# Kernel optimization log

Measured on AMD Instinct MI355X. Metric: run time of the kernel, lower is better.

The kernel has to match this reference:

```python
import jax, jax.numpy as jnp
import numpy as np

DIM = 1024
HEADS = 16
DIM_HEAD = 64
INNER = HEADS * DIM_HEAD
EPS = 1e-5

def layernorm(x, g, b):
    mu = jnp.mean(x, axis=-1, keepdims=True)
    var = jnp.var(x, axis=-1, keepdims=True)
    return (x - mu) * jax.lax.rsqrt(var + EPS) * g + b

def setup_inputs() -> dict:
    key = jax.random.key(0)
    ks = jax.random.split(key, 9)
    b, t, n, m = 8, 8, 576, 64
    x = jax.random.normal(ks[0], (b, t, n, DIM), dtype=jnp.float32)
    latents = jax.random.normal(ks[1], (b, t, m, DIM), dtype=jnp.float32)
    att_mask = jax.random.randint(ks[2], (b, t, n), 0, 2, dtype=jnp.int32)
    s = 1.0 / np.sqrt(DIM)
    Wq = jax.random.normal(ks[3], (DIM, INNER), dtype=jnp.float32) * s
    Wkv = jax.random.normal(ks[4], (DIM, 2 * INNER), dtype=jnp.float32) * s
    Wo = jax.random.normal(ks[5], (INNER, DIM), dtype=jnp.float32) * (1.0 / np.sqrt(INNER))
    gm = jnp.ones((DIM,), jnp.float32); bm = jnp.zeros((DIM,), jnp.float32)
    gl = jnp.ones((DIM,), jnp.float32); bl = jnp.zeros((DIM,), jnp.float32)
    return {"x": x, "latents": latents, "att_mask": att_mask,
            "gm": gm, "bm": bm, "gl": gl, "bl": bl,
            "Wq": Wq, "Wkv": Wkv, "Wo": Wo}

def reference(x, latents, att_mask, gm, bm, gl, bl, Wq, Wkv, Wo):
    b, t, n, d = x.shape
    m = latents.shape[2]
    h, dh = HEADS, DIM_HEAD
    scale = dh ** -0.5

    xn = layernorm(x, gm, bm)
    ln = layernorm(latents, gl, bl)

    q = ln @ Wq                                  # b t m inner
    kv_input = jnp.concatenate((xn, ln), axis=-2)  # b t (n+m) d
    kv = kv_input @ Wkv                          # b t (n+m) 2*inner
    k, v = jnp.split(kv, 2, axis=-1)

    # b t s (h dh) -> b h t s dh
    def split_heads(a):
        bb, tt, ss, _ = a.shape
        return a.reshape(bb, tt, ss, h, dh).transpose(0, 3, 1, 2, 4)
    q = split_heads(q) * scale
    k = split_heads(k)
    v = split_heads(v)

    sim = jnp.einsum('bhtid,bhtjd->bhtij', q, k)   # b h t m (n+m)

    # mask: concat ones for latent KV positions; broadcast over heads and query dim
    full_mask = jnp.concatenate(
        [att_mask.astype(sim.dtype), jnp.ones((b, t, m), sim.dtype)], axis=2)  # b t (n+m)
    neg = jnp.finfo(sim.dtype).min
    bias = jnp.where(full_mask > 0, 0.0, neg)      # b t (n+m)
    sim = sim + bias[:, None, :, None, :]

    attn = jax.nn.softmax(sim, axis=-1)
    out = jnp.einsum('bhtij,bhtjd->bhtid', attn, v)  # b h t m dh
    out = out.transpose(0, 2, 3, 1, 4).reshape(b, t, m, h * dh)
    return out @ Wo
```

## Files before the change

kernel.cpp:

```cpp
#include <hip/hip_runtime.h>
#include <hip/hip_bf16.h>
#include <stdint.h>

#define NCTX 576
#define MLAT 64
#define SEQ 640
#define DMODEL 1024
#define NH 16
#define INNER_ 1024
#define KV_W 2048

typedef float f32x4 __attribute__((ext_vector_type(4)));
typedef __bf16 bf16x8 __attribute__((ext_vector_type(8)));
typedef unsigned short u16;
typedef unsigned int u32;
typedef unsigned long long u64;

typedef __attribute__((address_space(1))) u32 as1_u32;
typedef __attribute__((address_space(3))) u32 as3_u32;

__device__ __forceinline__ u16 f2bf(float f) {
    u32 u = __builtin_bit_cast(u32, f);
    u32 r = (u + 0x7fffu + ((u >> 16) & 1u)) >> 16;
    return (u16)r;
}

__device__ __forceinline__ int xcd_swizzle(int orig, int nwg) {
    int q = nwg >> 3, r = nwg & 7;
    int xcd = orig & 7, loc = orig >> 3;
    return (xcd < r ? xcd * (q + 1) : r * (q + 1) + (xcd - r) * q) + loc;
}

__global__ __launch_bounds__(640) void build_idx(const int* __restrict__ mask,
                                                 int* __restrict__ sidx,
                                                 int* __restrict__ cnt,
                                                 int* __restrict__ latst) {
    int bt = blockIdx.x, tid = threadIdx.x;
    __shared__ int ps[640];
    int valid = (tid < NCTX) ? (mask[bt * NCTX + tid] > 0 ? 1 : 0) : 0;
    ps[tid] = valid;
    __syncthreads();
    for (int off = 1; off < 640; off <<= 1) {
        int v = (tid >= off) ? ps[tid - off] : 0;
        __syncthreads();
        ps[tid] += v;
        __syncthreads();
    }
    int nc = ps[NCTX - 1];
    if (valid) sidx[bt * SEQ + ps[tid] - 1] = tid;
    if (tid < MLAT) sidx[bt * SEQ + nc + tid] = NCTX + tid;
    if (tid == 0) { cnt[bt] = nc + MLAT; latst[bt] = nc; }
}

__global__ __launch_bounds__(256) void transpose_cast_all(const float* __restrict__ Wq,
                                                          const float* __restrict__ Wkv,
                                                          const float* __restrict__ Wo,
                                                          u16* __restrict__ WqT,
                                                          u16* __restrict__ WkvT,
                                                          u16* __restrict__ WoT) {
    __shared__ float tile[64][65];
    int id = blockIdx.x;
    const float* src; u16* dst; int N;
    if (id < 256)      { src = Wq;  dst = WqT;  N = 1024; }
    else if (id < 768) { src = Wkv; dst = WkvT; N = 2048; id -= 256; }
    else               { src = Wo;  dst = WoT;  N = 1024; id -= 768; }
    int nx = N >> 6;
    int n0 = (id % nx) * 64, k0 = (id / nx) * 64;
    int tid = threadIdx.x;
#pragma unroll
    for (int i = 0; i < 4; ++i) {
        int idx = i * 256 + tid;
        int kk = idx >> 4;
        int nn = (idx & 15) << 2;
        float4 v = *(const float4*)(src + (u64)(k0 + kk) * N + n0 + nn);
        tile[kk][nn] = v.x; tile[kk][nn + 1] = v.y; tile[kk][nn + 2] = v.z; tile[kk][nn + 3] = v.w;
    }
    __syncthreads();
#pragma unroll
    for (int i = 0; i < 4; ++i) {
        int idx = i * 256 + tid;
        int nn = idx >> 4;
        int kk = (idx & 15) << 2;
        ushort4 o;
        o.x = f2bf(tile[kk][nn]);     o.y = f2bf(tile[kk + 1][nn]);
        o.z = f2bf(tile[kk + 2][nn]); o.w = f2bf(tile[kk + 3][nn]);
        *(ushort4*)(dst + (u64)(n0 + nn) * 1024 + k0 + kk) = o;
    }
}

__global__ __launch_bounds__(256) void ln_cast(const float* __restrict__ x,
                                               const float* __restrict__ lat,
                                               const float* __restrict__ gm, const float* __restrict__ bm,
                                               const float* __restrict__ gl, const float* __restrict__ bl,
                                               u16* __restrict__ out,
                                               const int* __restrict__ sidx, const int* __restrict__ cnt,
                                               int bt0, int nrows) {
    int w = threadIdx.x >> 6, lane = threadIdx.x & 63;
    int nw = gridDim.x * 4;
    for (int row = blockIdx.x * 4 + w; row < nrows; row += nw) {
        int btl = row / SEQ, jl = row - btl * SEQ;
        int btg = bt0 + btl;
        if (jl >= cnt[btg]) continue;
        int sp = sidx[btg * SEQ + jl];
        const float *src, *g, *b;
        if (sp < NCTX) { src = x + ((u64)btl * NCTX + sp) * DMODEL; g = gm; b = bm; }
        else           { src = lat + ((u64)btl * MLAT + (sp - NCTX)) * DMODEL; g = gl; b = bl; }
        float4 v[4];
        float sum = 0.f, sq = 0.f;
#pragma unroll
        for (int j = 0; j < 4; ++j) {
            v[j] = *(const float4*)(src + ((j * 64 + lane) << 2));
            sum += v[j].x + v[j].y + v[j].z + v[j].w;
            sq  += v[j].x * v[j].x + v[j].y * v[j].y + v[j].z * v[j].z + v[j].w * v[j].w;
        }
#pragma unroll
        for (int off = 1; off < 64; off <<= 1) {
            sum += __shfl_xor(sum, off, 64);
            sq  += __shfl_xor(sq, off, 64);
        }
        float mu = sum * (1.0f / DMODEL);
        float var = sq * (1.0f / DMODEL) - mu * mu;
        float rstd = rsqrtf(var + 1e-5f);
        u16* orow = out + (u64)row * DMODEL;
#pragma unroll
        for (int j = 0; j < 4; ++j) {
            float4 gv = *(const float4*)(g + ((j * 64 + lane) << 2));
            float4 bv = *(const float4*)(b + ((j * 64 + lane) << 2));
            ushort4 o;
            o.x = f2bf((v[j].x - mu) * rstd * gv.x + bv.x);
            o.y = f2bf((v[j].y - mu) * rstd * gv.y + bv.y);
            o.z = f2bf((v[j].z - mu) * rstd * gv.z + bv.z);
            o.w = f2bf((v[j].w - mu) * rstd * gv.w + bv.w);
            *(ushort4*)(orow + ((j * 64 + lane) << 2)) = o;
        }
    }
}

template <int VT_SPLIT, typename OUT_T>
__global__ __launch_bounds__(512) void gemm256(const u16* __restrict__ A,
                                               const u16* __restrict__ Bt,
                                               OUT_T* __restrict__ C, u16* __restrict__ vt,
                                               int M, int ldc, float scale,
                                               const int* __restrict__ cntp, int bt0) {
    constexpr int K = 1024;
    constexpr int BK = 64;
    constexpr int NT = K / BK;
    __shared__ u16 As[2][256 * BK];
    __shared__ u16 Bs[2][256 * BK];
    int tid = threadIdx.x;
    int lane = tid & 63;
    int w = tid >> 6;
    int wm = w >> 2, wn = w & 3;
    int nwg = gridDim.x * gridDim.y;
    int wg = xcd_swizzle(blockIdx.y * gridDim.x + blockIdx.x, nwg);
    int m0 = (wg / gridDim.x) * 256;
    int n0 = (wg % gridDim.x) * 256;

    if (cntp) {
        int btile = m0 / SEQ, off = m0 - btile * SEQ;
        if (off + 256 <= SEQ && off >= cntp[bt0 + btile]) return;
    }

    int rl = lane & 15, cgl = lane >> 4;

    auto stage = [&](int t, int buf) {
        int k0 = t * BK;
#pragma unroll
        for (int i = 0; i < 4; ++i) {
            int r = i * 64 + (tid >> 3);
            int cg = tid & 7;
            int col = (cg ^ (r & 7)) << 3;
            __builtin_amdgcn_global_load_lds((const as1_u32*)(A + (u64)(m0 + r) * K + k0 + col),
                (as3_u32*)(&As[buf][0] + ((i * 512 + (w << 6)) << 3)), 16, 0, 0);
            __builtin_amdgcn_global_load_lds((const as1_u32*)(Bt + (u64)(n0 + r) * K + k0 + col),
                (as3_u32*)(&Bs[buf][0] + ((i * 512 + (w << 6)) << 3)), 16, 0, 0);
        }
    };

    f32x4 acc[8][4] = {};

    stage(0, 0);
    stage(1, 1);
    asm volatile("s_waitcnt vmcnt(8)" ::: "memory");
    __builtin_amdgcn_s_barrier();
    __builtin_amdgcn_sched_barrier(0);

#pragma unroll 1
    for (int t = 0; t < NT; ++t) {
        int buf = t & 1;
        const u16* Ab = &As[buf][0];
        const u16* Bb = &Bs[buf][0];
#pragma unroll
        for (int qd = 0; qd < 4; ++qd) {
            const int mh = qd & 1, nh = qd >> 1;
            bf16x8 a[2][4], b[2][2];
#pragma unroll
            for (int kk = 0; kk < 2; ++kk) {
#pragma unroll
                for (int mi = 0; mi < 4; ++mi) {
                    int r = wm * 128 + (mh * 4 + mi) * 16 + rl;
                    int c = kk * 4 + cgl;
                    a[kk][mi] = *(const bf16x8*)(Ab + r * BK + ((c ^ (r & 7)) << 3));
                }
#pragma unroll
                for (int ni = 0; ni < 2; ++ni) {
                    int r = wn * 64 + (nh * 2 + ni) * 16 + rl;
                    int c = kk * 4 + cgl;
                    b[kk][ni] = *(const bf16x8*)(Bb + r * BK + ((c ^ (r & 7)) << 3));
                }
            }
            __builtin_amdgcn_s_setprio(1);
#pragma unroll
            for (int kk = 0; kk < 2; ++kk)
#pragma unroll
                for (int mi = 0; mi < 4; ++mi)
#pragma unroll
                    for (int ni = 0; ni < 2; ++ni)
                        acc[mh * 4 + mi][nh * 2 + ni] = __builtin_amdgcn_mfma_f32_16x16x32_bf16(
                            a[kk][mi], b[kk][ni], acc[mh * 4 + mi][nh * 2 + ni], 0, 0, 0);
            __builtin_amdgcn_s_setprio(0);
        }
        __builtin_amdgcn_sched_barrier(0);
        __builtin_amdgcn_s_barrier();
        __builtin_amdgcn_sched_barrier(0);
        if (t + 2 < NT) {
            stage(t + 2, buf);
            asm volatile("s_waitcnt vmcnt(8)" ::: "memory");
        } else {
            asm volatile("s_waitcnt vmcnt(0)" ::: "memory");
        }
        __builtin_amdgcn_s_barrier();
        __builtin_amdgcn_sched_barrier(0);
    }

    if (VT_SPLIT && n0 >= INNER_) {
#pragma unroll
        for (int mi = 0; mi < 8; ++mi) {
            int grow = m0 + wm * 128 + mi * 16 + cgl * 4;
            int bt = grow / SEQ;
            int s = grow - bt * SEQ;
#pragma unroll
            for (int ni = 0; ni < 4; ++ni) {
                int vcol = (n0 - INNER_) + wn * 64 + ni * 16 + rl;
                ushort4 o;
                o.x = f2bf(acc[mi][ni][0] * scale);
                o.y = f2bf(acc[mi][ni][1] * scale);
                o.z = f2bf(acc[mi][ni][2] * scale);
                o.w = f2bf(acc[mi][ni][3] * scale);
                *(ushort4*)(vt + ((u64)bt * INNER_ + vcol) * SEQ + s) = o;
            }
        }
    } else {
#pragma unroll
        for (int mi = 0; mi < 8; ++mi) {
#pragma unroll
            for (int r = 0; r < 4; ++r) {
                int grow = m0 + wm * 128 + mi * 16 + cgl * 4 + r;
#pragma unroll
                for (int ni = 0; ni < 4; ++ni) {
                    int gcol = n0 + wn * 64 + ni * 16 + rl;
                    float val = acc[mi][ni][r] * scale;
                    if constexpr (sizeof(OUT_T) == 2)
                        C[(u64)grow * ldc + gcol] = (OUT_T)f2bf(val);
                    else
                        C[(u64)grow * ldc + gcol] = val;
                }
            }
        }
    }
}

template <typename OUT_T>
__global__ __launch_bounds__(256) void gemm_bf16(const u16* __restrict__ A,
                                                 const u16* __restrict__ Bt,
                                                 OUT_T* __restrict__ C,
                                                 int M, int ldc, float scale,
                                                 const int* __restrict__ latstart, int bt0) {
    constexpr int K = 1024;
    __shared__ u16 As[128 * 32];
    __shared__ u16 Bs[128 * 32];
    int tid = threadIdx.x;
    int lane = tid & 63;
    int w = tid >> 6;
    int wm = w >> 1, wn = w & 1;
    int nwg = gridDim.x * gridDim.y;
    int wg = xcd_swizzle(blockIdx.y * gridDim.x + blockIdx.x, nwg);
    int m0 = (wg / gridDim.x) * 128;
    int n0 = (wg % gridDim.x) * 128;

    f32x4 acc[4][4] = {};

    for (int k0 = 0; k0 < K; k0 += 32) {
        __syncthreads();
#pragma unroll
        for (int i = 0; i < 2; ++i) {
            int t = i * 256 + tid;
            int r = t >> 2;
            int cg = t & 3;
            int col = (cg ^ ((r >> 1) & 3)) << 3;
            int grow = m0 + r; if (grow >= M) grow = M - 1;
            u64 row;
            if (latstart) {
                int lbt = grow >> 6;
                row = (u64)lbt * SEQ + latstart[bt0 + lbt] + (grow & 63);
            } else {
                row = (u64)grow;
            }
            const u16* ga = A + row * K + k0 + col;
            __builtin_amdgcn_global_load_lds((const as1_u32*)ga,
                (as3_u32*)(As + ((i * 256 + (w << 6)) << 3)), 16, 0, 0);
            const u16* gb = Bt + (u64)(n0 + r) * K + k0 + col;
            __builtin_amdgcn_global_load_lds((const as1_u32*)gb,
                (as3_u32*)(Bs + ((i * 256 + (w << 6)) << 3)), 16, 0, 0);
        }
        __syncthreads();
        bf16x8 a[4], b[4];
        int rl = lane & 15;
        int cgl = lane >> 4;
#pragma unroll
        for (int mi = 0; mi < 4; ++mi) {
            int r = wm * 64 + mi * 16 + rl;
            int c = (cgl ^ ((r >> 1) & 3)) << 3;
            a[mi] = *(const bf16x8*)(As + r * 32 + c);
        }
#pragma unroll
        for (int ni = 0; ni < 4; ++ni) {
            int r = wn * 64 + ni * 16 + rl;
            int c = (cgl ^ ((r >> 1) & 3)) << 3;
            b[ni] = *(const bf16x8*)(Bs + r * 32 + c);
        }
#pragma unroll
        for (int mi = 0; mi < 4; ++mi)
#pragma unroll
            for (int ni = 0; ni < 4; ++ni)
                acc[mi][ni] = __builtin_amdgcn_mfma_f32_16x16x32_bf16(a[mi], b[ni], acc[mi][ni], 0, 0, 0);
    }
    int rl = lane & 15, rg = lane >> 4;
#pragma unroll
    for (int mi = 0; mi < 4; ++mi) {
#pragma unroll
        for (int r = 0; r < 4; ++r) {
            int grow = m0 + wm * 64 + mi * 16 + rg * 4 + r;
            if (grow < M) {
#pragma unroll
                for (int ni = 0; ni < 4; ++ni) {
                    int gcol = n0 + wn * 64 + ni * 16 + rl;
                    float val = acc[mi][ni][r] * scale;
                    if constexpr (sizeof(OUT_T) == 2)
                        C[(u64)grow * ldc + gcol] = (OUT_T)f2bf(val);
                    else
                        C[(u64)grow * ldc + gcol] = val;
                }
            }
        }
    }
}

__global__ __launch_bounds__(256) void attn_kernel(const u16* __restrict__ qb,
                                                   const u16* __restrict__ kbuf,
                                                   const u16* __restrict__ vtb,
                                                   const int* __restrict__ cnt,
                                                   u16* __restrict__ ob, int bt0) {
    int h = blockIdx.x;
    int btl = blockIdx.y;
    int tid = threadIdx.x, lane = tid & 63, w = tid >> 6;
    __shared__ u16 Ks[2][64 * 64];
    __shared__ u16 Vs[2][64 * 64];
    __shared__ u16 Ps[4][16 * 64];
    __shared__ float bias_s[2][64];
    int rl = lane & 15, cgl = lane >> 4;

    int cn = cnt[bt0 + btl];
    int nch = (cn + 63) >> 6;

    bf16x8 aq[2];
    {
        int qr = btl * MLAT + w * 16 + rl;
        const u16* qp = qb + (u64)qr * INNER_ + h * 64 + cgl * 8;
        aq[0] = *(const bf16x8*)(qp);
        aq[1] = *(const bf16x8*)(qp + 32);
    }
    f32x4 acc[4] = {};
    float mrow[4], lrow[4];
#pragma unroll
    for (int r = 0; r < 4; ++r) { mrow[r] = -1e30f; lrow[r] = 0.f; }

    const u16* kbase = kbuf + (u64)btl * SEQ * INNER_ + h * 64;
    const u16* vbase = vtb + ((u64)btl * INNER_ + h * 64) * SEQ;

    auto stage = [&](int c, int bf) {
#pragma unroll
        for (int i = 0; i < 2; ++i) {
            int t = i * 256 + tid;
            int r = t >> 3, cg = t & 7;
            int col = (cg ^ (r & 7)) << 3;
            __builtin_amdgcn_global_load_lds((const as1_u32*)(kbase + (u64)(c * 64 + r) * INNER_ + col),
                (as3_u32*)(&Ks[bf][0] + ((i * 256 + (w << 6)) << 3)), 16, 0, 0);
            __builtin_amdgcn_global_load_lds((const as1_u32*)(vbase + (u64)r * SEQ + c * 64 + col),
                (as3_u32*)(&Vs[bf][0] + ((i * 256 + (w << 6)) << 3)), 16, 0, 0);
        }
        if (tid < 64) {
            int pos = c * 64 + tid;
            bias_s[bf][tid] = (pos < cn) ? 0.f : -1e30f;
        }
    };

    stage(0, 0);
    __syncthreads();

    for (int c = 0; c < nch; ++c) {
        int bf = c & 1;
        if (c + 1 < nch) stage(c + 1, bf ^ 1);

        f32x4 sf[4];
        __builtin_amdgcn_s_setprio(1);
#pragma unroll
        for (int ni = 0; ni < 4; ++ni) {
            f32x4 z = {};
#pragma unroll
            for (int kk = 0; kk < 2; ++kk) {
                int r = ni * 16 + rl;
                int g = (kk * 4 + cgl) ^ (r & 7);
                bf16x8 bk = *(const bf16x8*)(&Ks[bf][0] + r * 64 + g * 8);
                z = __builtin_amdgcn_mfma_f32_16x16x32_bf16(aq[kk], bk, z, 0, 0, 0);
            }
            float bias = bias_s[bf][ni * 16 + rl];
            z[0] += bias; z[1] += bias; z[2] += bias; z[3] += bias;
            sf[ni] = z;
        }
        __builtin_amdgcn_s_setprio(0);
        float alpha[4];
#pragma unroll
        for (int r = 0; r < 4; ++r) {
            float m = fmaxf(fmaxf(sf[0][r], sf[1][r]), fmaxf(sf[2][r], sf[3][r]));
            m = fmaxf(m, __shfl_xor(m, 1, 64));
            m = fmaxf(m, __shfl_xor(m, 2, 64));
            m = fmaxf(m, __shfl_xor(m, 4, 64));
            m = fmaxf(m, __shfl_xor(m, 8, 64));
            float mn = fmaxf(mrow[r], m);
            alpha[r] = __expf(mrow[r] - mn);
            mrow[r] = mn;
        }
#pragma unroll
        for (int ni = 0; ni < 4; ++ni)
#pragma unroll
            for (int r = 0; r < 4; ++r)
                sf[ni][r] = __expf(sf[ni][r] - mrow[r]);
#pragma unroll
        for (int r = 0; r < 4; ++r) {
            float s = sf[0][r] + sf[1][r] + sf[2][r] + sf[3][r];
            s += __shfl_xor(s, 1, 64);
            s += __shfl_xor(s, 2, 64);
            s += __shfl_xor(s, 4, 64);
            s += __shfl_xor(s, 8, 64);
            lrow[r] = lrow[r] * alpha[r] + s;
        }
        u16* pw = Ps[w];
#pragma unroll
        for (int ni = 0; ni < 4; ++ni) {
#pragma unroll
            for (int r = 0; r < 4; ++r) {
                int qrow = cgl * 4 + r;
                int kcol = ni * 16 + rl;
                int cs = (((kcol >> 3) ^ (qrow & 7)) << 3) + (kcol & 7);
                pw[qrow * 64 + cs] = f2bf(sf[ni][r]);
            }
        }
#pragma unroll
        for (int oi = 0; oi < 4; ++oi)
#pragma unroll
            for (int r = 0; r < 4; ++r)
                acc[oi][r] *= alpha[r];
        bf16x8 ap[2];
#pragma unroll
        for (int kk = 0; kk < 2; ++kk) {
            int cc = (((kk * 4 + cgl) ^ (rl & 7)) << 3);
            ap[kk] = *(const bf16x8*)(pw + rl * 64 + cc);
        }
        __builtin_amdgcn_s_setprio(1);
#pragma unroll
        for (int oi = 0; oi < 4; ++oi) {
#pragma unroll
            for (int kk = 0; kk < 2; ++kk) {
                int r = oi * 16 + rl;
                int g = (kk * 4 + cgl) ^ (r & 7);
                bf16x8 bv = *(const bf16x8*)(&Vs[bf][0] + r * 64 + g * 8);
                acc[oi] = __builtin_amdgcn_mfma_f32_16x16x32_bf16(ap[kk], bv, acc[oi], 0, 0, 0);
            }
        }
        __builtin_amdgcn_s_setprio(0);
        __syncthreads();
    }
#pragma unroll
    for (int r = 0; r < 4; ++r) {
        float inv = 1.0f / lrow[r];
        int qrow = btl * MLAT + w * 16 + cgl * 4 + r;
        u16* op = ob + (u64)qrow * INNER_ + h * 64;
#pragma unroll
        for (int oi = 0; oi < 4; ++oi)
            op[oi * 16 + rl] = f2bf(acc[oi][r] * inv);
    }
}

extern "C" void kernel_launch(void* const* d_in, const int* in_sizes, int n_in,
                              void* d_out, int out_size, void* d_ws, size_t ws_size,
                              hipStream_t stream) {
    const float* x    = (const float*)d_in[0];
    const float* lat  = (const float*)d_in[1];
    const int*   am   = (const int*)d_in[2];
    const float* gm   = (const float*)d_in[3];
    const float* bm   = (const float*)d_in[4];
    const float* gl   = (const float*)d_in[5];
    const float* bl   = (const float*)d_in[6];
    const float* Wq   = (const float*)d_in[7];
    const float* Wkv  = (const float*)d_in[8];
    const float* Wo   = (const float*)d_in[9];
    float* out = (float*)d_out;

    int* sidx  = (int*)d_ws;
    int* cnt   = sidx + 64 * SEQ;
    int* latst = cnt + 64;
    u16* WqT   = (u16*)(latst + 64);
    u16* WkvT  = WqT + 1024 * 1024;
    u16* WoT   = WkvT + 2048 * 1024;
    u16* bufs  = WoT + 1024 * 1024;

    size_t fixed = (size_t)(64 * SEQ + 128) * 4 + (size_t)(1024 * 1024 + 2048 * 1024 + 1024 * 1024) * 2;
    size_t perbt = (size_t)(SEQ * DMODEL + SEQ * INNER_ + INNER_ * SEQ + MLAT * INNER_ + MLAT * INNER_) * 2;
    int C = 64;
    while (C > 1 && fixed + (size_t)C * perbt > ws_size) C >>= 1;

    build_idx<<<64, 640, 0, stream>>>(am, sidx, cnt, latst);
    transpose_cast_all<<<1024, 256, 0, stream>>>(Wq, Wkv, Wo, WqT, WkvT, WoT);

    for (int bt0 = 0; bt0 < 64; bt0 += C) {
        u16* xn  = bufs;
        u16* kb  = xn + (size_t)C * SEQ * DMODEL;
        u16* vtp = kb + (size_t)C * SEQ * INNER_;
        u16* qbp = vtp + (size_t)C * INNER_ * SEQ;
        u16* ao  = qbp + (size_t)C * MLAT * INNER_;

        ln_cast<<<2048, 256, 0, stream>>>(x + (u64)bt0 * NCTX * DMODEL,
                                          lat + (u64)bt0 * MLAT * DMODEL,
                                          gm, bm, gl, bl, xn, sidx, cnt, bt0, C * SEQ);
        gemm256<1, u16><<<dim3(KV_W / 256, (C * SEQ) / 256), 512, 0, stream>>>(
            xn, WkvT, kb, vtp, C * SEQ, INNER_, 1.0f, cnt, bt0);
        gemm_bf16<u16><<<dim3(INNER_ / 128, (C * MLAT) / 128), 256, 0, stream>>>(
            xn, WqT, qbp, C * MLAT, INNER_, 0.125f, latst, bt0);
        attn_kernel<<<dim3(NH, C), 256, 0, stream>>>(qbp, kb, vtp, cnt, ao, bt0);
        gemm_bf16<float><<<dim3(DMODEL / 128, (C * MLAT) / 128), 256, 0, stream>>>(
            ao, WoT, out + (u64)bt0 * MLAT * DMODEL, C * MLAT, DMODEL, 1.0f, nullptr, 0);
    }
}
```

Measured before the change: 499.9 us.

## Interleave KV GEMM tile loads with quadrant MFMA compute in finer-grained pipeline

Splits the per-k-step global-to-LDS staging of the KV projection GEMM into four sub-loads (two A halves, two B halves). Each sub-load is issued between the four MFMA quadrants, so the next tile's data streams in while the current tile is being computed. This replaces one bulk barrier-and-stage point per iteration. The rows written to a buffer are chosen so they are not read by the quadrants still pending, and adjusted vmcnt waits and barriers are placed at quadrant boundaries. The cost is more barriers per iteration and delicate buffer-hazard reasoning.

```diff
diff --git a/kernel.cpp b/kernel.cpp
--- a/kernel.cpp
+++ b/kernel.cpp
@@ -137,11 +137,11 @@
 }
 
 template <int VT_SPLIT, typename OUT_T>
-__global__ __launch_bounds__(512) void gemm256(const u16* __restrict__ A,
-                                               const u16* __restrict__ Bt,
-                                               OUT_T* __restrict__ C, u16* __restrict__ vt,
-                                               int M, int ldc, float scale,
-                                               const int* __restrict__ cntp, int bt0) {
+__global__ __launch_bounds__(512) void gemm256p(const u16* __restrict__ A,
+                                                const u16* __restrict__ Bt,
+                                                OUT_T* __restrict__ C, u16* __restrict__ vt,
+                                                int M, int ldc, float scale,
+                                                const int* __restrict__ cntp, int bt0) {
     constexpr int K = 1024;
     constexpr int BK = 64;
     constexpr int NT = K / BK;
@@ -162,76 +162,113 @@
     }
 
     int rl = lane & 15, cgl = lane >> 4;
-
-    auto stage = [&](int t, int buf) {
+    int col = ((tid & 7) ^ ((tid >> 3) & 7)) << 3;
+    int r0 = tid >> 3;
+
+    auto stAa = [&](int t, int bf) {
         int k0 = t * BK;
 #pragma unroll
-        for (int i = 0; i < 4; ++i) {
-            int r = i * 64 + (tid >> 3);
-            int cg = tid & 7;
-            int col = (cg ^ (r & 7)) << 3;
+        for (int j = 0; j < 2; ++j) {
+            int r = j * 128 + r0;
             __builtin_amdgcn_global_load_lds((const as1_u32*)(A + (u64)(m0 + r) * K + k0 + col),
-                (as3_u32*)(&As[buf][0] + ((i * 512 + (w << 6)) << 3)), 16, 0, 0);
+                (as3_u32*)(&As[bf][(j * 128 + w * 8) * BK]), 16, 0, 0);
+        }
+    };
+    auto stAb = [&](int t, int bf) {
+        int k0 = t * BK;
+#pragma unroll
+        for (int j = 0; j < 2; ++j) {
+            int r = j * 128 + 64 + r0;
+            __builtin_amdgcn_global_load_lds((const as1_u32*)(A + (u64)(m0 + r) * K + k0 + col),
+                (as3_u32*)(&As[bf][(j * 128 + 64 + w * 8) * BK]), 16, 0, 0);
+        }
+    };
+    auto stB0 = [&](int t, int bf) {
+        int k0 = t * BK;
+#pragma unroll
+        for (int j = 0; j < 2; ++j) {
+            int rb = (2 * j + (w >> 2)) * 64 + (w & 3) * 8;
+            int r = rb + ((tid >> 3) & 7);
             __builtin_amdgcn_global_load_lds((const as1_u32*)(Bt + (u64)(n0 + r) * K + k0 + col),
-                (as3_u32*)(&Bs[buf][0] + ((i * 512 + (w << 6)) << 3)), 16, 0, 0);
+                (as3_u32*)(&Bs[bf][rb * BK]), 16, 0, 0);
         }
     };
+    auto stB1 = [&](int t, int bf) {
+        int k0 = t * BK;
+#pragma unroll
+        for (int j = 0; j < 2; ++j) {
+            int rb = (2 * j + (w >> 2)) * 64 + 32 + (w & 3) * 8;
+            int r = rb + ((tid >> 3) & 7);
+            __builtin_amdgcn_global_load_lds((const as1_u32*)(Bt + (u64)(n0 + r) * K + k0 + col),
+                (as3_u32*)(&Bs[bf][rb * BK]), 16, 0, 0);
+        }
+    };
 
     f32x4 acc[8][4] = {};
 
-    stage(0, 0);
-    stage(1, 1);
-    asm volatile("s_waitcnt vmcnt(8)" ::: "memory");
-    __builtin_amdgcn_s_barrier();
-    __builtin_amdgcn_sched_barrier(0);
+#define FENCE() __builtin_amdgcn_sched_barrier(0); __builtin_amdgcn_s_barrier(); __builtin_amdgcn_sched_barrier(0)
+
+    stAa(0, 0); stAb(0, 0); stB0(0, 0); stB1(0, 0);
+    stAa(1, 1);
+    asm volatile("s_waitcnt vmcnt(2)" ::: "memory");
+    FENCE();
 
 #pragma unroll 1
     for (int t = 0; t < NT; ++t) {
-        int buf = t & 1;
-        const u16* Ab = &As[buf][0];
-        const u16* Bb = &Bs[buf][0];
-#pragma unroll
-        for (int qd = 0; qd < 4; ++qd) {
-            const int mh = qd & 1, nh = qd >> 1;
-            bf16x8 a[2][4], b[2][2];
-#pragma unroll
-            for (int kk = 0; kk < 2; ++kk) {
-#pragma unroll
-                for (int mi = 0; mi < 4; ++mi) {
-                    int r = wm * 128 + (mh * 4 + mi) * 16 + rl;
-                    int c = kk * 4 + cgl;
-                    a[kk][mi] = *(const bf16x8*)(Ab + r * BK + ((c ^ (r & 7)) << 3));
-                }
-#pragma unroll
-                for (int ni = 0; ni < 2; ++ni) {
-                    int r = wn * 64 + (nh * 2 + ni) * 16 + rl;
-                    int c = kk * 4 + cgl;
-                    b[kk][ni] = *(const bf16x8*)(Bb + r * BK + ((c ^ (r & 7)) << 3));
-                }
-            }
-            __builtin_amdgcn_s_setprio(1);
-#pragma unroll
-            for (int kk = 0; kk < 2; ++kk)
-#pragma unroll
-                for (int mi = 0; mi < 4; ++mi)
-#pragma unroll
-                    for (int ni = 0; ni < 2; ++ni)
-                        acc[mh * 4 + mi][nh * 2 + ni] = __builtin_amdgcn_mfma_f32_16x16x32_bf16(
-                            a[kk][mi], b[kk][ni], acc[mh * 4 + mi][nh * 2 + ni], 0, 0, 0);
-            __builtin_amdgcn_s_setprio(0);
-        }
-        __builtin_amdgcn_sched_barrier(0);
-        __builtin_amdgcn_s_barrier();
-        __builtin_amdgcn_sched_barrier(0);
-        if (t + 2 < NT) {
-            stage(t + 2, buf);
-            asm volatile("s_waitcnt vmcnt(8)" ::: "memory");
-        } else {
-            asm volatile("s_waitcnt vmcnt(0)" ::: "memory");
-        }
-        __builtin_amdgcn_s_barrier();
-        __builtin_amdgcn_sched_barrier(0);
-    }
+        int bf = t & 1;
+        const u16* Ab = &As[bf][0];
+        const u16* Bb = &Bs[bf][0];
+
+#define QUAD(MH, NH)                                                                     \
+        {                                                                                \
+            bf16x8 qa[2][4], qb[2][2];                                                   \
+            _Pragma("unroll")                                                            \
+            for (int kk = 0; kk < 2; ++kk) {                                             \
+                _Pragma("unroll")                                                        \
+                for (int mi = 0; mi < 4; ++mi) {                                         \
+                    int r = wm * 128 + ((MH) * 4 + mi) * 16 + rl;                        \
+                    qa[kk][mi] = *(const bf16x8*)(Ab + r * BK + (((kk * 4 + cgl) ^ (r & 7)) << 3)); \
+                }                                                                        \
+                _Pragma("unroll")                                                        \
+                for (int ni = 0; ni < 2; ++ni) {                                         \
+                    int r = wn * 64 + ((NH) * 2 + ni) * 16 + rl;                         \
+                    qb[kk][ni] = *(const bf16x8*)(Bb + r * BK + (((kk * 4 + cgl) ^ (r & 7)) << 3)); \
+                }                                                                        \
+            }                                                                            \
+            __builtin_amdgcn_s_setprio(1);                                               \
+            _Pragma("unroll")                                                            \
+            for (int kk = 0; kk < 2; ++kk)                                               \
+                _Pragma("unroll")                                                        \
+                for (int mi = 0; mi < 4; ++mi)                                           \
+                    _Pragma("unroll")                                                    \
+                    for (int ni = 0; ni < 2; ++ni)                                       \
+                        acc[(MH) * 4 + mi][(NH) * 2 + ni] =                              \
+                            __builtin_amdgcn_mfma_f32_16x16x32_bf16(                     \
+                                qa[kk][mi], qb[kk][ni], acc[(MH) * 4 + mi][(NH) * 2 + ni], 0, 0, 0); \
+            __builtin_amdgcn_s_setprio(0);                                               \
+        }
+
+        if (t + 1 < NT) stAb(t + 1, bf ^ 1);
+        QUAD(0, 0);
+        if (t == NT - 1) { asm volatile("s_waitcnt vmcnt(0)" ::: "memory"); }
+        else             { asm volatile("s_waitcnt vmcnt(2)" ::: "memory"); }
+        FENCE();
+
+        if (t + 1 < NT) stB0(t + 1, bf ^ 1);
+        QUAD(0, 1);
+        FENCE();
+
+        if (t + 2 < NT) stAa(t + 2, bf);
+        if (t + 1 < NT) stB1(t + 1, bf ^ 1);
+        QUAD(1, 0);
+        FENCE();
+
+        QUAD(1, 1);
+        asm volatile("s_waitcnt vmcnt(4)" ::: "memory");
+        FENCE();
+#undef QUAD
+    }
+#undef FENCE
 
     if (VT_SPLIT && n0 >= INNER_) {
 #pragma unroll
@@ -543,7 +580,7 @@
         ln_cast<<<2048, 256, 0, stream>>>(x + (u64)bt0 * NCTX * DMODEL,
                                           lat + (u64)bt0 * MLAT * DMODEL,
                                           gm, bm, gl, bl, xn, sidx, cnt, bt0, C * SEQ);
-        gemm256<1, u16><<<dim3(KV_W / 256, (C * SEQ) / 256), 512, 0, stream>>>(
+        gemm256p<1, u16><<<dim3(KV_W / 256, (C * SEQ) / 256), 512, 0, stream>>>(
             xn, WkvT, kb, vtp, C * SEQ, INNER_, 1.0f, cnt, bt0);
         gemm_bf16<u16><<<dim3(INNER_ / 128, (C * MLAT) / 128), 256, 0, stream>>>(
             xn, WqT, qbp, C * MLAT, INNER_, 0.125f, latst, bt0);
```

Result: slower. 547.4 us (+9.5%).
